# Kernel tuning notes

Hardware: AMD Instinct MI355X
Metric: run time of the kernel (lower is better)

Reference implementation:

```python
import jax, jax.numpy as jnp
import numpy as np

C, H, W = 512, 64, 64
N_PROP = 2000
ROI = 7          # roi_size
FEAT_STRIDE = 16
IMG = 1024.0
NEG = jnp.finfo(jnp.float32).min


def setup_inputs() -> dict:
    key = jax.random.key(0)
    k1, k2, k3, k4, k5 = jax.random.split(key, 5)
    features = jax.random.normal(k1, (1, C, H, W), dtype=jnp.float32)
    # proposals (x1, y1, x2, y2) in image pixel coords; width/height >= 32 px
    # so that after /feat_stride flooring each ROI spans >= 2 feature cells.
    x1 = jax.random.uniform(k2, (N_PROP,)) * (IMG - 64.0)
    y1 = jax.random.uniform(k3, (N_PROP,)) * (IMG - 64.0)
    bw = 32.0 + jax.random.uniform(k4, (N_PROP,)) * (IMG / 3.0)
    bh = 32.0 + jax.random.uniform(k5, (N_PROP,)) * (IMG / 3.0)
    x2 = jnp.minimum(x1 + bw, IMG - 1.0)
    y2 = jnp.minimum(y1 + bh, IMG - 1.0)
    proposals = jnp.stack([x1, y1, x2, y2], axis=1).astype(jnp.float32)
    return {"features": features, "proposals": proposals}


def _adaptive_bins(lo, length):
    # PyTorch AdaptiveMaxPool bin edges: start=floor(i*L/R), end=ceil((i+1)*L/R)
    i = jnp.arange(ROI)
    starts = lo + (i * length) // ROI
    ends = lo + ((i + 1) * length + ROI - 1) // ROI
    return starts, ends


def _pool_one(feats, prop):
    # prop: int32 [4] = (x1, y1, x2, y2) in feature-map coords
    x1, y1, x2, y2 = prop[0], prop[1], prop[2], prop[3]
    hs, he = _adaptive_bins(y1, y2 - y1)    # [ROI]
    ws, we = _adaptive_bins(x1, x2 - x1)    # [ROI]
    h_idx = jnp.arange(H)
    w_idx = jnp.arange(W)
    mask_h = (h_idx[None, :] >= hs[:, None]) & (h_idx[None, :] < he[:, None])  # [ROI,H]
    mask_w = (w_idx[None, :] >= ws[:, None]) & (w_idx[None, :] < we[:, None])  # [ROI,W]
    # stage 1: max over w per output column -> [C, H, ROI]
    t1 = jnp.max(jnp.where(mask_w[None, None, :, :], feats[:, :, None, :], NEG), axis=-1)
    # stage 2: max over h per output row -> [C, ROI, ROI]
    out = jnp.max(jnp.where(mask_h[None, :, :, None], t1[:, None, :, :], NEG), axis=2)
    return out


def reference(features, proposals):
    feats = jnp.squeeze(features, axis=0)                              # [C,H,W]
    props = jnp.floor(proposals / FEAT_STRIDE).astype(jnp.int32)       # [N,4]
    roi = jax.lax.map(lambda p: _pool_one(feats, p), props)            # [N,C,ROI,ROI]
    return roi.astype(jnp.float32)
```

## Files before the change

kernel.cpp:

```cpp
#include <hip/hip_runtime.h>


#define NCH   512
#define FH    64
#define FW    64
#define NPROP 2000
#define ROI   7
#define OUT_PER_PROP (NCH * ROI * ROI)
#define NCHUNK 4
#define CCH    128
#define TABE   (FH * FW * CCH)
#define TABG   (TABE / 4)
#define CHUNKG (4 * TABG)
#define TAB_BYTES ((size_t)NCHUNK * 4 * TABE * 2)
#define ROWG   (FW * (CCH / 4))

typedef float floatx4 __attribute__((ext_vector_type(4)));

__device__ __forceinline__ unsigned short f2bf(float f) {
    unsigned int u = __float_as_uint(f);
    u += 0x7fff + ((u >> 16) & 1);
    return (unsigned short)(u >> 16);
}

__device__ __forceinline__ void bf4max(uint2 u, float& a, float& b, float& c, float& d) {
    a = fmaxf(a, __uint_as_float(u.x << 16));
    b = fmaxf(b, __uint_as_float(u.x & 0xffff0000u));
    c = fmaxf(c, __uint_as_float(u.y << 16));
    d = fmaxf(d, __uint_as_float(u.y & 0xffff0000u));
}

__global__ __launch_bounds__(256) void prep2d_kernel(
    const float* __restrict__ f,
    unsigned short* __restrict__ ws)
{
    __shared__ float tA[64][65];
    __shared__ float tB[64][65];
    const int h  = blockIdx.x;
    const int g  = blockIdx.y;
    const int q  = g >> 1;
    const int cb = (g & 1) * 64;
    const int c0 = g * 64;
    const int h2 = min(h + 1, FH - 1);
    const int tw = threadIdx.x & 63;
    const int tg = threadIdx.x >> 6;
#pragma unroll
    for (int r = 0; r < 16; ++r) {
        const int cl = r * 4 + tg;
        tA[cl][tw] = f[(size_t)(c0 + cl) * (FH * FW) + h  * FW + tw];
        tB[cl][tw] = f[(size_t)(c0 + cl) * (FH * FW) + h2 * FW + tw];
    }
    __syncthreads();
    unsigned short* __restrict__ T = ws + (size_t)q * (4 * TABE);
#pragma unroll
    for (int r = 0; r < 16; ++r) {
        const int wl = r * 4 + tg;
        const int w1 = min(wl + 1, FW - 1);
        const float a0 = tA[tw][wl], a1 = tA[tw][w1];
        const float b0 = tB[tw][wl], b1 = tB[tw][w1];
        const float m01 = fmaxf(a0, a1);
        const float m10 = fmaxf(a0, b0);
        const float m11 = fmaxf(m01, fmaxf(b0, b1));
        const int o = (h * FW + wl) * CCH + cb + tw;
        T[o]            = f2bf(a0);
        T[TABE + o]     = f2bf(m01);
        T[2 * TABE + o] = f2bf(m10);
        T[3 * TABE + o] = f2bf(m11);
    }
}

template<bool H3, bool W3>
__device__ __forceinline__ void accum2d(
    const uint2* __restrict__ t2,
    int baseA, int baseB, int baseC,
    const int sA[ROI], const int sB[ROI], const int sC[ROI],
    float m0[ROI], float m1[ROI], float m2[ROI], float m3[ROI])
{
    const float NEG = -3.402823466e+38f;
    uint2 rAA[ROI], rAB[ROI], rBA[ROI], rBB[ROI];
#pragma unroll
    for (int j = 0; j < ROI; ++j) {
        rAA[j] = t2[(size_t)(baseA + sA[j])];
        rAB[j] = t2[(size_t)(baseA + sB[j])];
        rBA[j] = t2[(size_t)(baseB + sA[j])];
        rBB[j] = t2[(size_t)(baseB + sB[j])];
    }
#pragma unroll
    for (int j = 0; j < ROI; ++j) {
        float x0 = NEG, x1 = NEG, x2 = NEG, x3 = NEG;
        bf4max(rAA[j], x0, x1, x2, x3);
        bf4max(rAB[j], x0, x1, x2, x3);
        bf4max(rBA[j], x0, x1, x2, x3);
        bf4max(rBB[j], x0, x1, x2, x3);
        if (W3) {
            bf4max(t2[(size_t)(baseA + sC[j])], x0, x1, x2, x3);
            bf4max(t2[(size_t)(baseB + sC[j])], x0, x1, x2, x3);
        }
        if (H3) {
            bf4max(t2[(size_t)(baseC + sA[j])], x0, x1, x2, x3);
            bf4max(t2[(size_t)(baseC + sB[j])], x0, x1, x2, x3);
            if (W3) bf4max(t2[(size_t)(baseC + sC[j])], x0, x1, x2, x3);
        }
        m0[j] = x0; m1[j] = x1; m2[j] = x2; m3[j] = x3;
    }
}

__global__ __launch_bounds__(256, 4) void roipool_2d_kernel(
    const unsigned short* __restrict__ tabs,
    const float* __restrict__ props,
    float* __restrict__ out)
{
    const int b = blockIdx.x;
    const int q = b & 3;
    const int n = b >> 2;

    __shared__ __align__(16) float s_stage[CCH * 49];

    const float4 pv = ((const float4*)props)[n];
    const int x1 = (int)floorf(pv.x * 0.0625f);
    const int y1 = (int)floorf(pv.y * 0.0625f);
    const int x2 = (int)floorf(pv.z * 0.0625f);
    const int y2 = (int)floorf(pv.w * 0.0625f);
    const int Lh = y2 - y1;
    const int Lw = x2 - x1;

    int hs[ROI], he[ROI], wss[ROI], wee[ROI];
#pragma unroll
    for (int i = 0; i < ROI; ++i) {
        hs[i]  = max(y1 + (i * Lh) / ROI, 0);
        he[i]  = min(y1 + ((i + 1) * Lh + (ROI - 1)) / ROI, FH);
        wss[i] = max(x1 + (i * Lw) / ROI, 0);
        wee[i] = min(x1 + ((i + 1) * Lw + (ROI - 1)) / ROI, FW);
    }

    int sA[ROI], sB[ROI], sC[ROI];
    int w5f = 0, h5f = 0;
#pragma unroll
    for (int j = 0; j < ROI; ++j) {
        const int len = wee[j] - wss[j];
        const int kwo = (len >= 2) ? TABG : 0;
        const int wB  = (len >= 3) ? (wee[j] - 2) : wss[j];
        const int wC  = (len == 5) ? (wss[j] + 2) : wss[j];
        sA[j] = kwo + wss[j] * (CCH / 4);
        sB[j] = kwo + wB  * (CCH / 4);
        sC[j] = kwo + wC  * (CCH / 4);
        w5f |= (len == 5);
        h5f |= ((he[j] - hs[j]) == 5);
    }
    const bool w5 = __builtin_amdgcn_readfirstlane(w5f);
    const bool h5 = __builtin_amdgcn_readfirstlane(h5f);

    const int slot = threadIdx.x >> 5;
    const int bi   = min(slot, 6);
    const int c4   = threadIdx.x & 31;

    if (slot < 7) {
        int hsb = hs[0], heb = he[0];
#pragma unroll
        for (int i = 1; i < ROI; ++i) {
            if (bi == i) { hsb = hs[i]; heb = he[i]; }
        }
        const int hlen = heb - hsb;
        const int khoff = (hlen >= 2) ? (2 * TABG) : 0;
        const int hB   = (hlen >= 3) ? (heb - 2) : hsb;
        const int hC   = (hlen == 5) ? (hsb + 2) : hsb;

        const uint2* __restrict__ t2 = (const uint2*)tabs + (size_t)q * CHUNKG;
        const int baseA = khoff + hsb * ROWG + c4;
        const int baseB = khoff + hB  * ROWG + c4;
        const int baseC = khoff + hC  * ROWG + c4;

        float m0[ROI], m1[ROI], m2[ROI], m3[ROI];
        if (h5) {
            if (w5) accum2d<true,  true >(t2, baseA, baseB, baseC, sA, sB, sC, m0, m1, m2, m3);
            else    accum2d<true,  false>(t2, baseA, baseB, baseC, sA, sB, sC, m0, m1, m2, m3);
        } else {
            if (w5) accum2d<false, true >(t2, baseA, baseB, baseC, sA, sB, sC, m0, m1, m2, m3);
            else    accum2d<false, false>(t2, baseA, baseB, baseC, sA, sB, sC, m0, m1, m2, m3);
        }

#pragma unroll
        for (int j = 0; j < ROI; ++j) {
            s_stage[(4 * c4)     * 49 + bi * 7 + j] = m0[j];
            s_stage[(4 * c4 + 1) * 49 + bi * 7 + j] = m1[j];
            s_stage[(4 * c4 + 2) * 49 + bi * 7 + j] = m2[j];
            s_stage[(4 * c4 + 3) * 49 + bi * 7 + j] = m3[j];
        }
    }
    __syncthreads();

    floatx4* __restrict__ dsto = (floatx4*)(out + (size_t)n * OUT_PER_PROP + q * (CCH * 49));
    const floatx4* __restrict__ srco = (const floatx4*)s_stage;
    for (int i = threadIdx.x; i < (CCH * 49 / 4); i += 256)
        __builtin_nontemporal_store(srco[i], dsto + i);
}

__global__ __launch_bounds__(256) void roipool_direct_kernel(
    const float* __restrict__ feats,
    const float* __restrict__ props,
    float* __restrict__ out)
{
    const int n = blockIdx.x;
    __shared__ int s_hs[ROI], s_he[ROI], s_ws[ROI], s_we[ROI];
    if (threadIdx.x < ROI) {
        const int i = threadIdx.x;
        const int x1 = (int)floorf(props[n * 4 + 0] * 0.0625f);
        const int y1 = (int)floorf(props[n * 4 + 1] * 0.0625f);
        const int x2 = (int)floorf(props[n * 4 + 2] * 0.0625f);
        const int y2 = (int)floorf(props[n * 4 + 3] * 0.0625f);
        const int Lh = y2 - y1;
        const int Lw = x2 - x1;
        s_hs[i] = max(y1 + (i * Lh) / ROI, 0);
        s_he[i] = min(y1 + ((i + 1) * Lh + (ROI - 1)) / ROI, FH);
        s_ws[i] = max(x1 + (i * Lw) / ROI, 0);
        s_we[i] = min(x1 + ((i + 1) * Lw + (ROI - 1)) / ROI, FW);
    }
    __syncthreads();
    const float NEG = -3.402823466e+38f;
    const int base = blockIdx.y * (256 * ROI);
    float* outn = out + (size_t)n * OUT_PER_PROP;
#pragma unroll
    for (int k = 0; k < ROI; ++k) {
        const int idx = base + k * 256 + threadIdx.x;
        const int c   = idx / (ROI * ROI);
        const int bin = idx - c * (ROI * ROI);
        const int bi  = bin / ROI;
        const int bj  = bin - bi * ROI;
        float acc = NEG;
        for (int h = s_hs[bi]; h < s_he[bi]; ++h)
            for (int w = s_ws[bj]; w < s_we[bj]; ++w)
                acc = fmaxf(acc, feats[(size_t)c * (FH * FW) + h * FW + w]);
        outn[idx] = acc;
    }
}

extern "C" void kernel_launch(void* const* d_in, const int* in_sizes, int n_in,
                              void* d_out, int out_size, void* d_ws, size_t ws_size,
                              hipStream_t stream) {
    const float* feats = (const float*)d_in[0];
    const float* props = (const float*)d_in[1];
    float* out = (float*)d_out;

    if (ws_size >= TAB_BYTES) {
        unsigned short* ws = (unsigned short*)d_ws;
        prep2d_kernel<<<dim3(FH, NCH / 64), 256, 0, stream>>>(feats, ws);
        roipool_2d_kernel<<<dim3(NPROP * NCHUNK), 256, 0, stream>>>(ws, props, out);
    } else {
        roipool_direct_kernel<<<dim3(NPROP, ROI * 2), 256, 0, stream>>>(feats, props, out);
    }
}
```

Measured before the change: 57.97 us.

## Process all channel chunks per block with software-prefetched table loads

Each block now handles one proposal across all four channel chunks instead of one chunk per block, so the grid shrinks from 8000 to 2000 blocks. The next chunk's table loads are issued before the shared-memory staging and output store of the current chunk, which overlaps gather latency with stores and amortises the per-proposal bin setup. In exchange, each block adds two barriers per chunk and exposes less block-level parallelism, and the longer per-block serial loop may limit latency hiding.

```diff
diff --git a/kernel.cpp b/kernel.cpp
--- a/kernel.cpp
+++ b/kernel.cpp
@@ -70,38 +70,74 @@
 }
 
 template<bool H3, bool W3>
-__device__ __forceinline__ void accum2d(
+__device__ __forceinline__ void run_chunks(
     const uint2* __restrict__ t2,
     int baseA, int baseB, int baseC,
     const int sA[ROI], const int sB[ROI], const int sC[ROI],
-    float m0[ROI], float m1[ROI], float m2[ROI], float m3[ROI])
+    float* __restrict__ out_n,
+    float* __restrict__ s_stage,
+    int slot, int bi, int c4)
 {
     const float NEG = -3.402823466e+38f;
     uint2 rAA[ROI], rAB[ROI], rBA[ROI], rBB[ROI];
-#pragma unroll
-    for (int j = 0; j < ROI; ++j) {
-        rAA[j] = t2[(size_t)(baseA + sA[j])];
-        rAB[j] = t2[(size_t)(baseA + sB[j])];
-        rBA[j] = t2[(size_t)(baseB + sA[j])];
-        rBB[j] = t2[(size_t)(baseB + sB[j])];
-    }
-#pragma unroll
-    for (int j = 0; j < ROI; ++j) {
-        float x0 = NEG, x1 = NEG, x2 = NEG, x3 = NEG;
-        bf4max(rAA[j], x0, x1, x2, x3);
-        bf4max(rAB[j], x0, x1, x2, x3);
-        bf4max(rBA[j], x0, x1, x2, x3);
-        bf4max(rBB[j], x0, x1, x2, x3);
-        if (W3) {
-            bf4max(t2[(size_t)(baseA + sC[j])], x0, x1, x2, x3);
-            bf4max(t2[(size_t)(baseB + sC[j])], x0, x1, x2, x3);
+
+    if (slot < 7) {
+#pragma unroll
+        for (int j = 0; j < ROI; ++j) {
+            rAA[j] = t2[(size_t)(baseA + sA[j])];
+            rAB[j] = t2[(size_t)(baseA + sB[j])];
+            rBA[j] = t2[(size_t)(baseB + sA[j])];
+            rBB[j] = t2[(size_t)(baseB + sB[j])];
         }
-        if (H3) {
-            bf4max(t2[(size_t)(baseC + sA[j])], x0, x1, x2, x3);
-            bf4max(t2[(size_t)(baseC + sB[j])], x0, x1, x2, x3);
-            if (W3) bf4max(t2[(size_t)(baseC + sC[j])], x0, x1, x2, x3);
+    }
+
+#pragma unroll
+    for (int q = 0; q < NCHUNK; ++q) {
+        float m0[ROI], m1[ROI], m2[ROI], m3[ROI];
+        if (slot < 7) {
+            const size_t qo = (size_t)q * CHUNKG;
+#pragma unroll
+            for (int j = 0; j < ROI; ++j) {
+                float x0 = NEG, x1 = NEG, x2 = NEG, x3 = NEG;
+                bf4max(rAA[j], x0, x1, x2, x3);
+                bf4max(rAB[j], x0, x1, x2, x3);
+                bf4max(rBA[j], x0, x1, x2, x3);
+                bf4max(rBB[j], x0, x1, x2, x3);
+                if (W3) {
+                    bf4max(t2[qo + (baseA + sC[j])], x0, x1, x2, x3);
+                    bf4max(t2[qo + (baseB + sC[j])], x0, x1, x2, x3);
+                }
+                if (H3) {
+                    bf4max(t2[qo + (baseC + sA[j])], x0, x1, x2, x3);
+                    bf4max(t2[qo + (baseC + sB[j])], x0, x1, x2, x3);
+                    if (W3) bf4max(t2[qo + (baseC + sC[j])], x0, x1, x2, x3);
+                }
+                m0[j] = x0; m1[j] = x1; m2[j] = x2; m3[j] = x3;
+            }
+            if (q < NCHUNK - 1) {
+                const size_t qn = qo + CHUNKG;
+#pragma unroll
+                for (int j = 0; j < ROI; ++j) {
+                    rAA[j] = t2[qn + (baseA + sA[j])];
+                    rAB[j] = t2[qn + (baseA + sB[j])];
+                    rBA[j] = t2[qn + (baseB + sA[j])];
+                    rBB[j] = t2[qn + (baseB + sB[j])];
+                }
+            }
+#pragma unroll
+            for (int j = 0; j < ROI; ++j) {
+                s_stage[(4 * c4)     * 49 + bi * 7 + j] = m0[j];
+                s_stage[(4 * c4 + 1) * 49 + bi * 7 + j] = m1[j];
+                s_stage[(4 * c4 + 2) * 49 + bi * 7 + j] = m2[j];
+                s_stage[(4 * c4 + 3) * 49 + bi * 7 + j] = m3[j];
+            }
         }
-        m0[j] = x0; m1[j] = x1; m2[j] = x2; m3[j] = x3;
+        __syncthreads();
+        floatx4* __restrict__ dsto = (floatx4*)(out_n + q * (CCH * 49));
+        const floatx4* __restrict__ srco = (const floatx4*)s_stage;
+        for (int i = threadIdx.x; i < (CCH * 49 / 4); i += 256)
+            __builtin_nontemporal_store(srco[i], dsto + i);
+        __syncthreads();
     }
 }
 
@@ -110,10 +146,7 @@
     const float* __restrict__ props,
     float* __restrict__ out)
 {
-    const int b = blockIdx.x;
-    const int q = b & 3;
-    const int n = b >> 2;
-
+    const int n = blockIdx.x;
     __shared__ __align__(16) float s_stage[CCH * 49];
 
     const float4 pv = ((const float4*)props)[n];
@@ -154,45 +187,29 @@
     const int bi   = min(slot, 6);
     const int c4   = threadIdx.x & 31;
 
-    if (slot < 7) {
-        int hsb = hs[0], heb = he[0];
-#pragma unroll
-        for (int i = 1; i < ROI; ++i) {
-            if (bi == i) { hsb = hs[i]; heb = he[i]; }
-        }
-        const int hlen = heb - hsb;
-        const int khoff = (hlen >= 2) ? (2 * TABG) : 0;
-        const int hB   = (hlen >= 3) ? (heb - 2) : hsb;
-        const int hC   = (hlen == 5) ? (hsb + 2) : hsb;
-
-        const uint2* __restrict__ t2 = (const uint2*)tabs + (size_t)q * CHUNKG;
-        const int baseA = khoff + hsb * ROWG + c4;
-        const int baseB = khoff + hB  * ROWG + c4;
-        const int baseC = khoff + hC  * ROWG + c4;
-
-        float m0[ROI], m1[ROI], m2[ROI], m3[ROI];
-        if (h5) {
-            if (w5) accum2d<true,  true >(t2, baseA, baseB, baseC, sA, sB, sC, m0, m1, m2, m3);
-            else    accum2d<true,  false>(t2, baseA, baseB, baseC, sA, sB, sC, m0, m1, m2, m3);
-        } else {
-            if (w5) accum2d<false, true >(t2, baseA, baseB, baseC, sA, sB, sC, m0, m1, m2, m3);
-            else    accum2d<false, false>(t2, baseA, baseB, baseC, sA, sB, sC, m0, m1, m2, m3);
-        }
-
-#pragma unroll
-        for (int j = 0; j < ROI; ++j) {
-            s_stage[(4 * c4)     * 49 + bi * 7 + j] = m0[j];
-            s_stage[(4 * c4 + 1) * 49 + bi * 7 + j] = m1[j];
-            s_stage[(4 * c4 + 2) * 49 + bi * 7 + j] = m2[j];
-            s_stage[(4 * c4 + 3) * 49 + bi * 7 + j] = m3[j];
-        }
-    }
-    __syncthreads();
-
-    floatx4* __restrict__ dsto = (floatx4*)(out + (size_t)n * OUT_PER_PROP + q * (CCH * 49));
-    const floatx4* __restrict__ srco = (const floatx4*)s_stage;
-    for (int i = threadIdx.x; i < (CCH * 49 / 4); i += 256)
-        __builtin_nontemporal_store(srco[i], dsto + i);
+    int hsb = hs[0], heb = he[0];
+#pragma unroll
+    for (int i = 1; i < ROI; ++i) {
+        if (bi == i) { hsb = hs[i]; heb = he[i]; }
+    }
+    const int hlen = heb - hsb;
+    const int khoff = (hlen >= 2) ? (2 * TABG) : 0;
+    const int hB   = (hlen >= 3) ? (heb - 2) : hsb;
+    const int hC   = (hlen == 5) ? (hsb + 2) : hsb;
+
+    const uint2* __restrict__ t2 = (const uint2*)tabs;
+    const int baseA = khoff + hsb * ROWG + c4;
+    const int baseB = khoff + hB  * ROWG + c4;
+    const int baseC = khoff + hC  * ROWG + c4;
+
+    float* out_n = out + (size_t)n * OUT_PER_PROP;
+    if (h5) {
+        if (w5) run_chunks<true,  true >(t2, baseA, baseB, baseC, sA, sB, sC, out_n, s_stage, slot, bi, c4);
+        else    run_chunks<true,  false>(t2, baseA, baseB, baseC, sA, sB, sC, out_n, s_stage, slot, bi, c4);
+    } else {
+        if (w5) run_chunks<false, true >(t2, baseA, baseB, baseC, sA, sB, sC, out_n, s_stage, slot, bi, c4);
+        else    run_chunks<false, false>(t2, baseA, baseB, baseC, sA, sB, sC, out_n, s_stage, slot, bi, c4);
+    }
 }
 
 __global__ __launch_bounds__(256) void roipool_direct_kernel(
@@ -244,7 +261,7 @@
     if (ws_size >= TAB_BYTES) {
         unsigned short* ws = (unsigned short*)d_ws;
         prep2d_kernel<<<dim3(FH, NCH / 64), 256, 0, stream>>>(feats, ws);
-        roipool_2d_kernel<<<dim3(NPROP * NCHUNK), 256, 0, stream>>>(ws, props, out);
+        roipool_2d_kernel<<<dim3(NPROP), 256, 0, stream>>>(ws, props, out);
     } else {
         roipool_direct_kernel<<<dim3(NPROP, ROI * 2), 256, 0, stream>>>(feats, props, out);
     }
```

Result: slower. 65.48 us (+12.9%).
